# Optimization experiments

Measured on AMD Instinct MI355X. Metric: run time of the kernel, lower is better.

Reference implementation:

```python
import jax, jax.numpy as jnp
import numpy as np

H = 16       # num query heads
KV = 4       # num kv heads
D = 64       # head_dim
EPS = 1e-6


def setup_inputs() -> dict:
    key = jax.random.key(0)
    ks = jax.random.split(key, 12)
    B, N, E = 2, 2048, 1024
    s = 0.02
    return {
        "x": jax.random.normal(ks[0], (B, N, E), jnp.float32),
        "sin": jax.random.normal(ks[1], (N, D), jnp.float32),
        "cos": jax.random.normal(ks[2], (N, D), jnp.float32),
        "wq_w": jax.random.normal(ks[3], (E, E), jnp.float32) * s,
        "wq_b": jax.random.normal(ks[4], (E,), jnp.float32) * s,
        "wk_w": jax.random.normal(ks[5], (KV * D, E), jnp.float32) * s,
        "wk_b": jax.random.normal(ks[6], (KV * D,), jnp.float32) * s,
        "wv_w": jax.random.normal(ks[7], (KV * D, E), jnp.float32) * s,
        "wv_b": jax.random.normal(ks[8], (KV * D,), jnp.float32) * s,
        "qn_w": jnp.ones((D,), jnp.float32),
        "kn_w": jnp.ones((D,), jnp.float32),
        "proj_w": jax.random.normal(ks[9], (E, E), jnp.float32) * s,
        "proj_b": jax.random.normal(ks[10], (E,), jnp.float32) * s,
    }


def _rmsnorm(t, w):
    # t: [..., D]
    var = jnp.mean(t * t, axis=-1, keepdims=True)
    return t * jax.lax.rsqrt(var + EPS) * w


def _rope(t, sin, cos):
    # t: [B,h,N,D]; sin/cos: [N,D] broadcast
    x1, x2 = jnp.split(t, 2, axis=-1)
    rotated = jnp.concatenate([-x2, x1], axis=-1)
    return t * cos + rotated * sin


def reference(x, sin, cos, wq_w, wq_b, wk_w, wk_b, wv_w, wv_b,
              qn_w, kn_w, proj_w, proj_b):
    B, N, E = x.shape
    q = (x @ wq_w.T + wq_b).reshape(B, N, H, D).transpose(0, 2, 1, 3)   # [B,H,N,D]
    k = (x @ wk_w.T + wk_b).reshape(B, N, KV, D).transpose(0, 2, 1, 3)  # [B,KV,N,D]
    v = (x @ wv_w.T + wv_b).reshape(B, N, KV, D).transpose(0, 2, 1, 3)
    q = _rmsnorm(q, qn_w)
    k = _rmsnorm(k, kn_w)
    # GQA: repeat kv heads to match query heads (repeat_interleave on head dim)
    factor = H // KV
    k = jnp.repeat(k, factor, axis=1)  # [B,H,N,D]
    v = jnp.repeat(v, factor, axis=1)
    # RoPE (n_extra = 0 since sin covers full sequence)
    q = _rope(q, sin, cos)
    k = _rope(k, sin, cos)
    # scaled dot-product attention
    scale = 1.0 / np.sqrt(D).astype(np.float32)
    scores = jnp.einsum("bhqd,bhkd->bhqk", q, k) * scale
    attn = jax.nn.softmax(scores, axis=-1)
    out = jnp.einsum("bhqk,bhkd->bhqd", attn, v)      # [B,H,N,D]
    out = out.transpose(0, 2, 1, 3).reshape(B, N, E)  # [B,N,E]
    return out @ proj_w.T + proj_b
```

## Files before the change

kernel.cpp:

```cpp
#include <hip/hip_runtime.h>
#include <hip/hip_bf16.h>
#include <math.h>


#define N_SEQ 2048
#define EMB   1024
#define NH    16
#define NKV   4
#define HD    64
#define BATCH 2
#define M_TOT 4096
#define QKV_N 1536

typedef __attribute__((ext_vector_type(8)))  short short8;
typedef __attribute__((ext_vector_type(4)))  float f32x4;
typedef __attribute__((ext_vector_type(16))) float f32x16;

__device__ __forceinline__ ushort f2bf(float f) {
    union { __hip_bfloat16 h; ushort u; } cv;
    cv.h = __float2bfloat16(f);
    return cv.u;
}
__device__ __forceinline__ float bf2f(ushort u) {
    union { __hip_bfloat16 h; ushort u; } cv;
    cv.u = u;
    return __bfloat162float(cv.h);
}
__device__ __forceinline__ uint pack2bf(float a, float b) {
    union { __hip_bfloat162 h; uint u; } cv;
    cv.h = __float22bfloat162_rn(float2{a, b});
    return cv.u;
}

__device__ __forceinline__ void cvt4(const float* __restrict__ s,
                                     ushort* __restrict__ d, long g, long gd) {
    const float4 v = ((const float4*)s)[g];
    ushort4 o;
    o.x = f2bf(v.x); o.y = f2bf(v.y); o.z = f2bf(v.z); o.w = f2bf(v.w);
    ((ushort4*)d)[gd] = o;
}

__global__ __launch_bounds__(256) void prep_kernel(
    const float* __restrict__ x,  const float* __restrict__ wq,
    const float* __restrict__ wk, const float* __restrict__ wv,
    const float* __restrict__ wp, const float* __restrict__ bq,
    const float* __restrict__ bk, const float* __restrict__ bv,
    ushort* __restrict__ xb, ushort* __restrict__ Wqkv,
    ushort* __restrict__ Wproj, float* __restrict__ bqkv)
{
    const long i = (long)blockIdx.x * 256 + threadIdx.x;
    if (i < 1048576) {
        cvt4(x, xb, i, i);
    } else if (i < 1310720) {
        const long g = i - 1048576;
        cvt4(wq, Wqkv, g, g);
    } else if (i < 1376256) {
        const long g = i - 1310720;
        cvt4(wk, Wqkv, g, 262144 + g);
    } else if (i < 1441792) {
        const long g = i - 1376256;
        cvt4(wv, Wqkv, g, 327680 + g);
    } else if (i < 1703936) {
        const long g = i - 1441792;
        cvt4(wp, Wproj, g, g);
    } else if (i < 1704320) {
        const long j = i - 1703936;
        float4 v;
        if (j < 256)      v = ((const float4*)bq)[j];
        else if (j < 320) v = ((const float4*)bk)[j - 256];
        else              v = ((const float4*)bv)[j - 320];
        ((float4*)bqkv)[j] = v;
    }
}

template <bool BF16OUT>
__global__ __launch_bounds__(256) void gemm_mfma_kernel(
    const ushort* __restrict__ A, const ushort* __restrict__ W,
    const float* __restrict__ bias, void* __restrict__ Cout,
    int K, int ldc)
{
    __shared__ ushort As[128 * 40];
    __shared__ ushort Bs[64 * 40];

    const int tid = threadIdx.x;
    const int m0 = blockIdx.y * 128, n0 = blockIdx.x * 64;
    const int w = tid >> 6, lane = tid & 63;
    const int quad = lane >> 4, l16 = lane & 15;
    const int wm = w * 32;

    f32x4 acc[2][4] = {};

    float bb[4];
#pragma unroll
    for (int j = 0; j < 4; ++j) bb[j] = bias[n0 + j * 16 + l16];

    const int r0 = tid >> 2;
    const int c0 = tid & 3;
    const ushort* Ap = A + (size_t)(m0 + r0) * K + c0 * 8;
    const ushort* Wp = W + (size_t)(n0 + r0) * K + c0 * 8;

    for (int k0 = 0; k0 < K; k0 += 32) {
        const short8 a0 = *(const short8*)(Ap + k0);
        const short8 a1 = *(const short8*)(Ap + (size_t)64 * K + k0);
        const short8 b0 = *(const short8*)(Wp + k0);
        __syncthreads();
        *(short8*)&As[r0 * 40 + c0 * 8] = a0;
        *(short8*)&As[(r0 + 64) * 40 + c0 * 8] = a1;
        *(short8*)&Bs[r0 * 40 + c0 * 8] = b0;
        __syncthreads();

        short8 aF[2], bF[4];
#pragma unroll
        for (int i = 0; i < 2; ++i)
            aF[i] = *(const short8*)&As[(wm + i * 16 + l16) * 40 + quad * 8];
#pragma unroll
        for (int j = 0; j < 4; ++j)
            bF[j] = *(const short8*)&Bs[(j * 16 + l16) * 40 + quad * 8];
        __builtin_amdgcn_s_setprio(1);
#pragma unroll
        for (int i = 0; i < 2; ++i)
#pragma unroll
            for (int j = 0; j < 4; ++j)
                acc[i][j] = __builtin_amdgcn_mfma_f32_16x16x32_bf16(
                    aF[i], bF[j], acc[i][j], 0, 0, 0);
        __builtin_amdgcn_s_setprio(0);
    }

#pragma unroll
    for (int i = 0; i < 2; ++i) {
        const int rowb = m0 + wm + i * 16 + quad * 4;
#pragma unroll
        for (int j = 0; j < 4; ++j) {
            const int col = n0 + j * 16 + l16;
#pragma unroll
            for (int r = 0; r < 4; ++r) {
                const float vv = acc[i][j][r] + bb[j];
                if (BF16OUT)
                    ((ushort*)Cout)[(size_t)(rowb + r) * ldc + col] = f2bf(vv);
                else
                    ((float*)Cout)[(size_t)(rowb + r) * ldc + col] = vv;
            }
        }
    }
}

__global__ __launch_bounds__(256) void norm_rope_kernel(
    const ushort* __restrict__ Tq, const float* __restrict__ qn_w,
    const float* __restrict__ kn_w, const float* __restrict__ sinp,
    const float* __restrict__ cosp, ushort* __restrict__ Qb,
    ushort* __restrict__ Kf)
{
    const int gw = (int)(((long)blockIdx.x * 256 + threadIdx.x) >> 6);
    const int lane = threadIdx.x & 63;

    const bool isQ = (gw < 65536);
    const int vec = isQ ? gw : gw - 65536;
    const int hshift = isQ ? 4 : 2;
    const int colBase = isQ ? 0 : EMB;
    const float* nw = isQ ? qn_w : kn_w;
    const float outScale = isQ ? 0.125f : 1.0f;

    const int m = vec >> hshift;
    const int h = vec & ((1 << hshift) - 1);
    const int n = m & (N_SEQ - 1);
    const int b = m >> 11;

    const float t = bf2f(Tq[(size_t)m * QKV_N + colBase + h * HD + lane]);
    float s = t * t;
#pragma unroll
    for (int mask = 32; mask; mask >>= 1) s += __shfl_xor(s, mask, 64);
    const float r = rsqrtf(s * (1.0f / 64.0f) + 1e-6f);

    const float tn = t * r * nw[lane];
    const float partner = __shfl_xor(tn, 32, 64);
    const float rot = (lane < 32) ? -partner : partner;
    const float val = (tn * cosp[n * HD + lane] + rot * sinp[n * HD + lane]) * outScale;

    if (isQ) {
        Qb[((size_t)((b << 4) + h) * N_SEQ + n) * HD + lane] = f2bf(val);
    } else {
        const int kt = n >> 6, rr = n & 63, ss = rr >> 5, l32k = rr & 31;
        const int c = lane >> 4, l5k = (lane >> 3) & 1, j = lane & 7;
        Kf[((size_t)(b * NKV + h) * 32 + kt) * 4096
           + (ss * 4 + c) * 512 + l32k * 16 + l5k * 8 + j] = f2bf(val);
    }
}

__global__ __launch_bounds__(256) void transpose_v_kernel(
    const ushort* __restrict__ Tq, ushort* __restrict__ Vf)
{
    __shared__ ushort L[64 * 72];
    const int kt = blockIdx.x;
    const int n0 = kt * 64;
    const int bkv = blockIdx.y;
    const int b = bkv >> 2, kv = bkv & 3;
    const int tid = threadIdx.x;

#pragma unroll
    for (int it = 0; it < 2; ++it) {
        const int j = tid + it * 256;
        const int r = j >> 3, c = j & 7;
        const short8 v = *(const short8*)&Tq[(size_t)(b * N_SEQ + n0 + r) * QKV_N
                                             + 1280 + kv * HD + c * 8];
        *(short8*)&L[r * 72 + c * 8] = v;
    }
    __syncthreads();
#pragma unroll
    for (int it = 0; it < 2; ++it) {
        const int j = tid + it * 256;
        const int d = j >> 3, c8 = j & 7;
        short8 o;
#pragma unroll
        for (int e = 0; e < 8; ++e) o[e] = (short)L[(c8 * 8 + e) * 72 + d];
        const int ss = c8 >> 2, tt = (c8 >> 1) & 1, l5v = c8 & 1;
        const int d2 = d >> 5, l32v = d & 31;
        *(short8*)&Vf[((size_t)bkv * 32 + kt) * 4096
                      + ((ss * 2 + tt) * 2 + d2) * 512 + l32v * 16 + l5v * 8] = o;
    }
}

__global__ __launch_bounds__(256, 4) void flash_mfma32_kernel(
    const ushort* __restrict__ Qb, const ushort* __restrict__ Kf,
    const ushort* __restrict__ Vf, ushort* __restrict__ Ob)
{
    __shared__ float fsm[4352];

    const int qt = blockIdx.x;
    const int bh = blockIdx.y;
    const int b = bh >> 4, h = bh & 15;
    const int kvh = h >> 2;
    const int tid = threadIdx.x;
    const int w = tid >> 6, lane = tid & 63;
    const int l32 = lane & 31, l5 = lane >> 5;
    const int qg = w & 1;
    const int kh = w >> 1;

    const ushort* Qg = Qb + ((size_t)bh * N_SEQ + qt * 64 + qg * 32) * HD;
    const size_t kvbase = (size_t)(b * NKV + kvh) * (32 * 4096);
    const ushort* Kp = Kf + kvbase;
    const ushort* Vp = Vf + kvbase;
    const int loff = l32 * 16 + l5 * 8;

    short8 qF[4];
#pragma unroll
    for (int c = 0; c < 4; ++c)
        qF[c] = *(const short8*)&Qg[(size_t)l32 * HD + c * 16 + l5 * 8];

    f32x16 Oa[2] = {};
    float mrow = -3.0e38f, lrow = 0.0f;

    for (int i = 0; i < 16; ++i) {
        const int kt = kh * 16 + i;
        const ushort* Kt = Kp + kt * 4096;
        const ushort* Vt = Vp + kt * 4096;

        short8 kT[2][4];
#pragma unroll
        for (int s = 0; s < 2; ++s)
#pragma unroll
            for (int c = 0; c < 4; ++c)
                kT[s][c] = *(const short8*)&Kt[(s * 4 + c) * 512 + loff];
        short8 vT[2][2][2];
#pragma unroll
        for (int s = 0; s < 2; ++s)
#pragma unroll
            for (int t = 0; t < 2; ++t)
#pragma unroll
                for (int d2 = 0; d2 < 2; ++d2)
                    vT[s][t][d2] = *(const short8*)&Vt[((s * 2 + t) * 2 + d2) * 512 + loff];

        f32x16 Sv[2] = {};
#pragma unroll
        for (int s = 0; s < 2; ++s)
#pragma unroll
            for (int c = 0; c < 4; ++c)
                Sv[s] = __builtin_amdgcn_mfma_f32_32x32x16_bf16(kT[s][c], qF[c], Sv[s], 0, 0, 0);

        float mx = -3.0e38f;
#pragma unroll
        for (int s = 0; s < 2; ++s)
#pragma unroll
            for (int r = 0; r < 16; ++r) mx = fmaxf(mx, Sv[s][r]);
        mx = fmaxf(mx, __shfl_xor(mx, 32, 64));
        const float mnew = fmaxf(mrow, mx);
        const float alpha = __expf(mrow - mnew);
        mrow = mnew;
        float rs = 0.0f;
#pragma unroll
        for (int s = 0; s < 2; ++s)
#pragma unroll
            for (int r = 0; r < 16; ++r) {
                Sv[s][r] = __expf(Sv[s][r] - mnew);
                rs += Sv[s][r];
            }
        rs += __shfl_xor(rs, 32, 64);
        lrow = lrow * alpha + rs;
#pragma unroll
        for (int t = 0; t < 2; ++t)
#pragma unroll
            for (int r = 0; r < 16; ++r) Oa[t][r] *= alpha;

        uint P2[2][8];
#pragma unroll
        for (int s = 0; s < 2; ++s)
#pragma unroll
            for (int g = 0; g < 4; ++g)
#pragma unroll
                for (int hh = 0; hh < 2; ++hh)
                    P2[s][g * 2 + hh] =
                        pack2bf(Sv[s][4 * g + 2 * hh], Sv[s][4 * g + 2 * hh + 1]);

#pragma unroll
        for (int s = 0; s < 2; ++s)
#pragma unroll
            for (int t = 0; t < 2; ++t) {
                const uint snd0 = l5 ? P2[s][4 * t + 0] : P2[s][4 * t + 2];
                const uint snd1 = l5 ? P2[s][4 * t + 1] : P2[s][4 * t + 3];
                const uint kp0  = l5 ? P2[s][4 * t + 2] : P2[s][4 * t + 0];
                const uint kp1  = l5 ? P2[s][4 * t + 3] : P2[s][4 * t + 1];
                const uint rcv0 = __shfl_xor(snd0, 32, 64);
                const uint rcv1 = __shfl_xor(snd1, 32, 64);
                union { uint u[4]; short8 s8; } pb;
                pb.u[0] = l5 ? rcv0 : kp0;
                pb.u[1] = l5 ? rcv1 : kp1;
                pb.u[2] = l5 ? kp0 : rcv0;
                pb.u[3] = l5 ? kp1 : rcv1;
#pragma unroll
                for (int d2 = 0; d2 < 2; ++d2)
                    Oa[d2] = __builtin_amdgcn_mfma_f32_32x32x16_bf16(
                        vT[s][t][d2], pb.s8, Oa[d2], 0, 0, 0);
            }
    }

    float* buf = fsm + qg * 2176;
    if (kh == 1) {
#pragma unroll
        for (int d2 = 0; d2 < 2; ++d2)
#pragma unroll
            for (int r = 0; r < 16; ++r)
                buf[(d2 * 16 + r) * 64 + lane] = Oa[d2][r];
        buf[2048 + lane] = mrow;
        buf[2112 + lane] = lrow;
    }
    __syncthreads();

    if (kh == 0) {
        const float mb = buf[2048 + lane];
        const float lb = buf[2112 + lane];
        const float M = fmaxf(mrow, mb);
        const float ea = __expf(mrow - M), eb = __expf(mb - M);
        lrow = lrow * ea + lb * eb;
#pragma unroll
        for (int d2 = 0; d2 < 2; ++d2)
#pragma unroll
            for (int r = 0; r < 16; ++r)
                Oa[d2][r] = Oa[d2][r] * ea + buf[(d2 * 16 + r) * 64 + lane] * eb;
    }
    __syncthreads();

    ushort* Os = (ushort*)fsm;
    if (kh == 0) {
        const float inv = 1.0f / lrow;
#pragma unroll
        for (int d2 = 0; d2 < 2; ++d2)
#pragma unroll
            for (int r = 0; r < 16; ++r) {
                const int d = d2 * 32 + (r & 3) + 8 * (r >> 2) + 4 * l5;
                Os[(qg * 32 + l32) * 68 + d] = f2bf(Oa[d2][r] * inv);
            }
    }
    __syncthreads();

    const int row = tid >> 2, cc = (tid & 3) * 16;
#pragma unroll
    for (int i = 0; i < 2; ++i) {
        const short8 v = *(const short8*)&Os[row * 68 + cc + i * 8];
        *(short8*)&Ob[((size_t)b * N_SEQ + qt * 64 + row) * EMB + h * HD + cc + i * 8] = v;
    }
}

extern "C" void kernel_launch(void* const* d_in, const int* in_sizes, int n_in,
                              void* d_out, int out_size, void* d_ws, size_t ws_size,
                              hipStream_t stream)
{
    const float* x      = (const float*)d_in[0];
    const float* sinp   = (const float*)d_in[1];
    const float* cosp   = (const float*)d_in[2];
    const float* wq_w   = (const float*)d_in[3];
    const float* wq_b   = (const float*)d_in[4];
    const float* wk_w   = (const float*)d_in[5];
    const float* wk_b   = (const float*)d_in[6];
    const float* wv_w   = (const float*)d_in[7];
    const float* wv_b   = (const float*)d_in[8];
    const float* qn_w   = (const float*)d_in[9];
    const float* kn_w   = (const float*)d_in[10];
    const float* proj_w = (const float*)d_in[11];
    const float* proj_b = (const float*)d_in[12];
    float* out = (float*)d_out;

    ushort* Tq    = (ushort*)d_ws;
    ushort* xb    = Tq + 6291456;
    ushort* Wqkv  = xb + 4194304;
    ushort* Wproj = Wqkv + 1572864;
    float*  bqkv  = (float*)(Wproj + 1048576);
    ushort* Qb    = (ushort*)(bqkv + 1536);
    ushort* Kf    = Qb + 4194304;
    ushort* Vf    = Kf + 1048576;

    prep_kernel<<<6658, 256, 0, stream>>>(x, wq_w, wk_w, wv_w, proj_w,
                                          wq_b, wk_b, wv_b,
                                          xb, Wqkv, Wproj, bqkv);

    gemm_mfma_kernel<true><<<dim3(QKV_N / 64, M_TOT / 128), 256, 0, stream>>>(
        xb, Wqkv, bqkv, Tq, EMB, QKV_N);

    norm_rope_kernel<<<20480, 256, 0, stream>>>(Tq, qn_w, kn_w, sinp, cosp, Qb, Kf);

    transpose_v_kernel<<<dim3(32, 8), 256, 0, stream>>>(Tq, Vf);

    flash_mfma32_kernel<<<dim3(32, 32), 256, 0, stream>>>(Qb, Kf, Vf, xb);

    gemm_mfma_kernel<false><<<dim3(EMB / 64, M_TOT / 128), 256, 0, stream>>>(
        xb, Wproj, proj_b, out, EMB, EMB);
}
```

Measured before the change: 220.5 us.

## Fuse RMSNorm and RoPE into the QKV GEMM epilogue

```diff
diff --git a/kernel.cpp b/kernel.cpp
--- a/kernel.cpp
+++ b/kernel.cpp
@@ -73,11 +73,13 @@
     }
 }
 
-template <bool BF16OUT>
-__global__ __launch_bounds__(256) void gemm_mfma_kernel(
+__global__ __launch_bounds__(256) void gemm_qkv_fused(
     const ushort* __restrict__ A, const ushort* __restrict__ W,
-    const float* __restrict__ bias, void* __restrict__ Cout,
-    int K, int ldc)
+    const float* __restrict__ bias,
+    const float* __restrict__ qn_w, const float* __restrict__ kn_w,
+    const float* __restrict__ sinp, const float* __restrict__ cosp,
+    ushort* __restrict__ Qb, ushort* __restrict__ Kf,
+    ushort* __restrict__ Tq)
 {
     __shared__ ushort As[128 * 40];
     __shared__ ushort Bs[64 * 40];
@@ -87,6 +89,7 @@
     const int w = tid >> 6, lane = tid & 63;
     const int quad = lane >> 4, l16 = lane & 15;
     const int wm = w * 32;
+    const int K = EMB;
 
     f32x4 acc[2][4] = {};
 
@@ -126,6 +129,133 @@
         __builtin_amdgcn_s_setprio(0);
     }
 
+    if (n0 < 1280) {
+        const bool isQ = (n0 < 1024);
+        const float* nw = isQ ? qn_w : kn_w;
+        const float oscale = isQ ? 0.125f : 1.0f;
+        float nwv[4];
+#pragma unroll
+        for (int j = 0; j < 4; ++j) nwv[j] = nw[j * 16 + l16];
+
+#pragma unroll
+        for (int i = 0; i < 2; ++i) {
+#pragma unroll
+            for (int r = 0; r < 4; ++r) {
+                const int m = m0 + wm + i * 16 + quad * 4 + r;
+                const int n = m & (N_SEQ - 1);
+                const int bI = m >> 11;
+
+                float v4[4];
+                float ssum = 0.0f;
+#pragma unroll
+                for (int j = 0; j < 4; ++j) {
+                    v4[j] = acc[i][j][r] + bb[j];
+                    ssum += v4[j] * v4[j];
+                }
+                ssum += __shfl_xor(ssum, 1, 64);
+                ssum += __shfl_xor(ssum, 2, 64);
+                ssum += __shfl_xor(ssum, 4, 64);
+                ssum += __shfl_xor(ssum, 8, 64);
+                const float rinv = rsqrtf(ssum * (1.0f / 64.0f) + 1e-6f);
+
+                float tn[4], val[4];
+#pragma unroll
+                for (int j = 0; j < 4; ++j) tn[j] = v4[j] * rinv * nwv[j];
+#pragma unroll
+                for (int j = 0; j < 4; ++j) {
+                    const int d = j * 16 + l16;
+                    const float rot = (j < 2) ? -tn[j + 2] : tn[j - 2];
+                    val[j] = (tn[j] * cosp[n * HD + d] + rot * sinp[n * HD + d]) * oscale;
+                }
+
+                if (isQ) {
+                    const size_t qrow =
+                        ((size_t)((bI << 4) + (n0 >> 6)) * N_SEQ + n) * HD;
+#pragma unroll
+                    for (int j = 0; j < 4; ++j)
+                        Qb[qrow + j * 16 + l16] = f2bf(val[j]);
+                } else {
+                    const int kvh = (n0 >> 6) - 16;
+                    const int kt = n >> 6, rr = n & 63;
+                    const int ss2 = rr >> 5, l32k = rr & 31;
+                    const size_t kb =
+                        ((size_t)(bI * NKV + kvh) * 32 + kt) * 4096 + l32k * 16 + l16;
+#pragma unroll
+                    for (int j = 0; j < 4; ++j)
+                        Kf[kb + (ss2 * 4 + j) * 512] = f2bf(val[j]);
+                }
+            }
+        }
+    } else {
+#pragma unroll
+        for (int i = 0; i < 2; ++i) {
+            const int rowb = m0 + wm + i * 16 + quad * 4;
+#pragma unroll
+            for (int j = 0; j < 4; ++j) {
+                const int col = n0 + j * 16 + l16;
+#pragma unroll
+                for (int r = 0; r < 4; ++r) {
+                    const float vv = acc[i][j][r] + bb[j];
+                    Tq[(size_t)(rowb + r) * QKV_N + col] = f2bf(vv);
+                }
+            }
+        }
+    }
+}
+
+template <bool BF16OUT>
+__global__ __launch_bounds__(256) void gemm_mfma_kernel(
+    const ushort* __restrict__ A, const ushort* __restrict__ W,
+    const float* __restrict__ bias, void* __restrict__ Cout,
+    int K, int ldc)
+{
+    __shared__ ushort As[128 * 40];
+    __shared__ ushort Bs[64 * 40];
+
+    const int tid = threadIdx.x;
+    const int m0 = blockIdx.y * 128, n0 = blockIdx.x * 64;
+    const int w = tid >> 6, lane = tid & 63;
+    const int quad = lane >> 4, l16 = lane & 15;
+    const int wm = w * 32;
+
+    f32x4 acc[2][4] = {};
+
+    float bb[4];
+#pragma unroll
+    for (int j = 0; j < 4; ++j) bb[j] = bias[n0 + j * 16 + l16];
+
+    const int r0 = tid >> 2;
+    const int c0 = tid & 3;
+    const ushort* Ap = A + (size_t)(m0 + r0) * K + c0 * 8;
+    const ushort* Wp = W + (size_t)(n0 + r0) * K + c0 * 8;
+
+    for (int k0 = 0; k0 < K; k0 += 32) {
+        const short8 a0 = *(const short8*)(Ap + k0);
+        const short8 a1 = *(const short8*)(Ap + (size_t)64 * K + k0);
+        const short8 b0 = *(const short8*)(Wp + k0);
+        __syncthreads();
+        *(short8*)&As[r0 * 40 + c0 * 8] = a0;
+        *(short8*)&As[(r0 + 64) * 40 + c0 * 8] = a1;
+        *(short8*)&Bs[r0 * 40 + c0 * 8] = b0;
+        __syncthreads();
+
+        short8 aF[2], bF[4];
+#pragma unroll
+        for (int i = 0; i < 2; ++i)
+            aF[i] = *(const short8*)&As[(wm + i * 16 + l16) * 40 + quad * 8];
+#pragma unroll
+        for (int j = 0; j < 4; ++j)
+            bF[j] = *(const short8*)&Bs[(j * 16 + l16) * 40 + quad * 8];
+        __builtin_amdgcn_s_setprio(1);
+#pragma unroll
+        for (int i = 0; i < 2; ++i)
+#pragma unroll
+            for (int j = 0; j < 4; ++j)
+                acc[i][j] = __builtin_amdgcn_mfma_f32_16x16x32_bf16(
+                    aF[i], bF[j], acc[i][j], 0, 0, 0);
+        __builtin_amdgcn_s_setprio(0);
+    }
+
 #pragma unroll
     for (int i = 0; i < 2; ++i) {
         const int rowb = m0 + wm + i * 16 + quad * 4;
@@ -141,48 +271,6 @@
                     ((float*)Cout)[(size_t)(rowb + r) * ldc + col] = vv;
             }
         }
-    }
-}
-
-__global__ __launch_bounds__(256) void norm_rope_kernel(
-    const ushort* __restrict__ Tq, const float* __restrict__ qn_w,
-    const float* __restrict__ kn_w, const float* __restrict__ sinp,
-    const float* __restrict__ cosp, ushort* __restrict__ Qb,
-    ushort* __restrict__ Kf)
-{
-    const int gw = (int)(((long)blockIdx.x * 256 + threadIdx.x) >> 6);
-    const int lane = threadIdx.x & 63;
-
-    const bool isQ = (gw < 65536);
-    const int vec = isQ ? gw : gw - 65536;
-    const int hshift = isQ ? 4 : 2;
-    const int colBase = isQ ? 0 : EMB;
-    const float* nw = isQ ? qn_w : kn_w;
-    const float outScale = isQ ? 0.125f : 1.0f;
-
-    const int m = vec >> hshift;
-    const int h = vec & ((1 << hshift) - 1);
-    const int n = m & (N_SEQ - 1);
-    const int b = m >> 11;
-
-    const float t = bf2f(Tq[(size_t)m * QKV_N + colBase + h * HD + lane]);
-    float s = t * t;
-#pragma unroll
-    for (int mask = 32; mask; mask >>= 1) s += __shfl_xor(s, mask, 64);
-    const float r = rsqrtf(s * (1.0f / 64.0f) + 1e-6f);
-
-    const float tn = t * r * nw[lane];
-    const float partner = __shfl_xor(tn, 32, 64);
-    const float rot = (lane < 32) ? -partner : partner;
-    const float val = (tn * cosp[n * HD + lane] + rot * sinp[n * HD + lane]) * outScale;
-
-    if (isQ) {
-        Qb[((size_t)((b << 4) + h) * N_SEQ + n) * HD + lane] = f2bf(val);
-    } else {
-        const int kt = n >> 6, rr = n & 63, ss = rr >> 5, l32k = rr & 31;
-        const int c = lane >> 4, l5k = (lane >> 3) & 1, j = lane & 7;
-        Kf[((size_t)(b * NKV + h) * 32 + kt) * 4096
-           + (ss * 4 + c) * 512 + l32k * 16 + l5k * 8 + j] = f2bf(val);
     }
 }
 
@@ -411,10 +499,8 @@
                                           wq_b, wk_b, wv_b,
                                           xb, Wqkv, Wproj, bqkv);
 
-    gemm_mfma_kernel<true><<<dim3(QKV_N / 64, M_TOT / 128), 256, 0, stream>>>(
-        xb, Wqkv, bqkv, Tq, EMB, QKV_N);
-
-    norm_rope_kernel<<<20480, 256, 0, stream>>>(Tq, qn_w, kn_w, sinp, cosp, Qb, Kf);
+    gemm_qkv_fused<<<dim3(QKV_N / 64, M_TOT / 128), 256, 0, stream>>>(
+        xb, Wqkv, bqkv, qn_w, kn_w, sinp, cosp, Qb, Kf, Tq);
 
     transpose_v_kernel<<<dim3(32, 8), 256, 0, stream>>>(Tq, Vf);
 
```

After: 208.2 us. 1.06x faster.
